# Kernel tuning notes

Hardware: AMD Instinct MI355X
Metric: run time of the kernel (lower is better)

## Reference

```python
import jax, jax.numpy as jnp
import numpy as np

L, H, E, DK, FF, V, BS = 6, 16, 1024, 64, 4096, 32000, 1024
B, T = 2, 1024
EPS = 1e-5


def _ln(x, g, b):
    mu = jnp.mean(x, axis=-1, keepdims=True)
    var = jnp.mean(jnp.square(x - mu), axis=-1, keepdims=True)
    return (x - mu) * jax.lax.rsqrt(var + EPS) * g + b


def setup_inputs() -> dict:
    key = jax.random.key(0)
    ks = jax.random.split(key, 12)
    s = 0.02
    return {
        'idx': jax.random.randint(ks[0], (B, T), 0, V),
        'emb': jax.random.normal(ks[1], (V, E), jnp.float32) * s,
        'pos': jax.random.normal(ks[2], (BS, E), jnp.float32) * s,
        'Wq': jax.random.normal(ks[3], (L, H, E, DK), jnp.float32) * s,
        'Wk': jax.random.normal(ks[4], (L, H, E, DK), jnp.float32) * s,
        'Wv': jax.random.normal(ks[5], (L, H, E, DK), jnp.float32) * s,
        'Wp': jax.random.normal(ks[6], (L, E, E), jnp.float32) * s,
        'bp': jnp.zeros((L, E), jnp.float32),
        'ln1_g': jnp.ones((L, E), jnp.float32),
        'ln1_b': jnp.zeros((L, E), jnp.float32),
        'ln2_g': jnp.ones((L, E), jnp.float32),
        'ln2_b': jnp.zeros((L, E), jnp.float32),
        'W1': jax.random.normal(ks[7], (L, E, FF), jnp.float32) * s,
        'b1': jnp.zeros((L, FF), jnp.float32),
        'W2': jax.random.normal(ks[8], (L, FF, E), jnp.float32) * s,
        'b2': jnp.zeros((L, E), jnp.float32),
        'lnf_g': jnp.ones((E,), jnp.float32),
        'lnf_b': jnp.zeros((E,), jnp.float32),
        'Wout': jax.random.normal(ks[9], (E, V), jnp.float32) * s,
        'bout': jnp.zeros((V,), jnp.float32),
    }


def reference(idx, emb, pos, Wq, Wk, Wv, Wp, bp, ln1_g, ln1_b, ln2_g, ln2_b,
              W1, b1, W2, b2, lnf_g, lnf_b, Wout, bout):
    Tcur = idx.shape[1]
    x = emb[idx] + pos[:Tcur]  # [B,T,E]
    # NOTE: original code scales by 1/sqrt(n_embd) (input dim), NOT 1/sqrt(d_k)
    scale = 1.0 / jnp.sqrt(jnp.float32(E))
    causal = jnp.tril(jnp.ones((Tcur, Tcur), bool))
    neg_inf = jnp.float32(-jnp.inf)
    for l in range(L):
        h = _ln(x, ln1_g[l], ln1_b[l])
        q = jnp.einsum('bte,hed->bhtd', h, Wq[l])
        k = jnp.einsum('bte,hed->bhtd', h, Wk[l])
        v = jnp.einsum('bte,hed->bhtd', h, Wv[l])
        scores = jnp.einsum('bhtd,bhsd->bhts', q, k) * scale
        scores = jnp.where(causal, scores, neg_inf)
        attn = jax.nn.softmax(scores, axis=-1)
        o = jnp.einsum('bhts,bhsd->bhtd', attn, v)
        o = o.transpose(0, 2, 1, 3).reshape(x.shape[0], Tcur, H * DK)
        x = x + o @ Wp[l] + bp[l]
        h = _ln(x, ln2_g[l], ln2_b[l])
        x = x + jax.nn.relu(h @ W1[l] + b1[l]) @ W2[l] + b2[l]
    x = _ln(x, lnf_g, lnf_b)
    logits = x @ Wout + bout  # [B,T,V]
    return logits
```

## Files before the change

### kernel.cpp

```cpp
#include <hip/hip_runtime.h>
#include <cstdio>
#include <cstdint>

typedef unsigned short u16;
typedef __bf16 bf16x8 __attribute__((ext_vector_type(8)));
typedef float f32x4 __attribute__((ext_vector_type(4)));

static const int EE = 1024;
static const int TT = 1024;
static const int BB = 2;
static const int NTOK = 2048;
static const int HH = 16;
static const int DK = 64;
static const int FF = 4096;
static const int VV = 32000;
static const int LL = 6;

__device__ __forceinline__ float bf2f(u16 u) {
  unsigned int i = ((unsigned int)u) << 16;
  float f; __builtin_memcpy(&f, &i, 4); return f;
}
__device__ __forceinline__ u16 f2bf(float f) {
  unsigned int i; __builtin_memcpy(&i, &f, 4);
  unsigned int r = i + 0x7fffu + ((i >> 16) & 1u);
  return (u16)(r >> 16);
}

__device__ __forceinline__ void gll16(const u16* g, u16* l) {
  __builtin_amdgcn_global_load_lds(
      (__attribute__((address_space(1))) void*)(uintptr_t)g,
      (__attribute__((address_space(3))) void*)l,
      16, 0, 0);
}

__global__ __launch_bounds__(256) void embed_k(const int* __restrict__ idx,
                                               const float* __restrict__ emb,
                                               const float* __restrict__ pos,
                                               float* __restrict__ x) {
  long i = (long)blockIdx.x * 256 + threadIdx.x;
  int n = (int)(i >> 10), e = (int)(i & 1023);
  int tok = idx[n];
  int t = n & (TT - 1);
  x[i] = emb[(long)tok * EE + e] + pos[(long)t * EE + e];
}

template <int NS>
__global__ __launch_bounds__(256) void ln_fused_k(float* __restrict__ x,
                                                  const float* __restrict__ part, long pstride,
                                                  const float* __restrict__ bias,
                                                  const float* __restrict__ g,
                                                  const float* __restrict__ b,
                                                  u16* __restrict__ out) {
  int row = blockIdx.x * 4 + (threadIdx.x >> 6);
  int lane = threadIdx.x & 63;
  long base = (long)row * EE;
  float v[16];
  float s = 0.f, s2 = 0.f;
#pragma unroll
  for (int j = 0; j < 16; j++) {
    int c = j * 64 + lane;
    float t = x[base + c];
    if constexpr (NS > 0) {
      t += bias[c];
#pragma unroll
      for (int p = 0; p < NS; p++) t += part[(long)p * pstride + base + c];
      x[base + c] = t;
    }
    v[j] = t; s += t; s2 += t * t;
  }
#pragma unroll
  for (int o = 32; o; o >>= 1) { s += __shfl_xor(s, o); s2 += __shfl_xor(s2, o); }
  float mu = s * (1.f / EE);
  float var = s2 * (1.f / EE) - mu * mu;
  float rs = rsqrtf(var + 1e-5f);
  u16* orow = out + base;
#pragma unroll
  for (int j = 0; j < 16; j++) {
    int c = j * 64 + lane;
    orow[c] = f2bf((v[j] - mu) * rs * g[c] + b[c]);
  }
}

__global__ __launch_bounds__(256) void pack_qkvT_k(const float* __restrict__ Wq,
                                                   const float* __restrict__ Wk,
                                                   const float* __restrict__ Wv,
                                                   u16* __restrict__ out) {
  int l = blockIdx.y;
  const float* Wq_l = Wq + (size_t)l * HH * EE * DK;
  const float* Wk_l = Wk + (size_t)l * HH * EE * DK;
  const float* Wv_l = Wv + (size_t)l * HH * EE * DK;
  u16* out_l = out + (size_t)l * 3 * EE * EE;
  long base = ((long)blockIdx.x * 256 + threadIdx.x) * 4;
  int c = (int)(base >> 10);
  int e0 = (int)(base & 1023);
  const float* W = (c < 1024) ? Wq_l : (c < 2048 ? Wk_l : Wv_l);
  int cm = c & 1023;
  int hh = cm >> 6, d = cm & 63;
#pragma unroll
  for (int i = 0; i < 4; i++) {
    int e = e0 + i;
    out_l[(long)c * EE + e] = f2bf(W[((long)hh * EE + e) * DK + d]);
  }
}

template <typename ST>
__global__ __launch_bounds__(256) void transpose_to_bf16(const ST* __restrict__ src,
                                                         long s_z1, long s_z2, int zmod, int ld_s,
                                                         u16* __restrict__ dst,
                                                         long d_z, int ld_d, int R, int C) {
  __shared__ u16 t[32][33];
  int z = blockIdx.z;
  const ST* S = src + (z / zmod) * s_z1 + (z % zmod) * s_z2;
  u16* D = dst + (long)z * d_z;
  int c0 = blockIdx.x * 32, r0 = blockIdx.y * 32;
  int lx = threadIdx.x & 31, ly = threadIdx.x >> 5;
#pragma unroll
  for (int i = 0; i < 4; i++) {
    int r = r0 + ly + i * 8;
    ST val = S[(long)r * ld_s + c0 + lx];
    if constexpr (sizeof(ST) == 4) t[ly + i * 8][lx] = f2bf((float)val);
    else t[ly + i * 8][lx] = (u16)val;
  }
  __syncthreads();
#pragma unroll
  for (int i = 0; i < 4; i++) {
    int c = c0 + ly + i * 8;
    D[(long)c * ld_d + r0 + lx] = t[lx][ly + i * 8];
  }
}

__global__ __launch_bounds__(256) void flash_attn_k(const u16* __restrict__ qkv,
                                                    const u16* __restrict__ vT,
                                                    u16* __restrict__ o) {
  __shared__ u16 Qs[64 * 72];
  __shared__ u16 Ks[2][64 * 72];
  __shared__ u16 Vs[2][64 * 72];
  __shared__ u16 Ps[4][16 * 72];

  int tid = threadIdx.x;
  int lane = tid & 63, w = tid >> 6;
  int fr = lane & 15, kg = lane >> 4;
  int z = blockIdx.y;
  int b = z >> 4, h = z & 15;
  const u16* qbase = qkv + (long)b * TT * 3072 + h * 64;
  const u16* kbase = qbase + 1024;
  const u16* vbase = vT + (long)z * DK * TT;
  const float scale = 0.03125f;

  for (int p = 0; p < 2; p++) {
    int jq = (p == 0) ? (int)blockIdx.x : 15 - (int)blockIdx.x;
    int q0 = jq * 64;
    int nt = jq + 1;
    if (p) __syncthreads();

    int4 kreg[2], vreg[2];
#pragma unroll
    for (int i = 0; i < 2; i++) {
      int c = i * 256 + tid, row = c >> 3, c8 = c & 7;
      *(int4*)&Qs[row * 72 + c8 * 8] = *(const int4*)(qbase + (long)(q0 + row) * 3072 + c8 * 8);
      kreg[i] = *(const int4*)(kbase + (long)row * 3072 + c8 * 8);
      vreg[i] = *(const int4*)(vbase + (long)row * TT + c8 * 8);
    }
#pragma unroll
    for (int i = 0; i < 2; i++) {
      int c = i * 256 + tid, row = c >> 3, c8 = c & 7;
      *(int4*)&Ks[0][row * 72 + c8 * 8] = kreg[i];
      *(int4*)&Vs[0][row * 72 + c8 * 8] = vreg[i];
    }
    __syncthreads();

    f32x4 zero = {0.f, 0.f, 0.f, 0.f};
    f32x4 acc_o[4];
    float m_i[4], l_i[4];
#pragma unroll
    for (int n = 0; n < 4; n++) acc_o[n] = zero;
#pragma unroll
    for (int r = 0; r < 4; r++) { m_i[r] = -1e30f; l_i[r] = 0.f; }

    for (int t = 0; t < nt; t++) {
      int cur = t & 1;
      int kv0 = t * 64;
      bool pf = (t + 1 < nt);
      if (pf) {
        int kvn = kv0 + 64;
#pragma unroll
        for (int i = 0; i < 2; i++) {
          int c = i * 256 + tid, row = c >> 3, c8 = c & 7;
          kreg[i] = *(const int4*)(kbase + (long)(kvn + row) * 3072 + c8 * 8);
          vreg[i] = *(const int4*)(vbase + (long)row * TT + kvn + c8 * 8);
        }
      }

      f32x4 s[4];
#pragma unroll
      for (int n = 0; n < 4; n++) s[n] = zero;
      {
        bf16x8 aq[2], bk[4][2];
#pragma unroll
        for (int kk = 0; kk < 2; kk++)
          aq[kk] = *(const bf16x8*)&Qs[(w * 16 + fr) * 72 + kk * 32 + kg * 8];
#pragma unroll
        for (int n = 0; n < 4; n++)
#pragma unroll
          for (int kk = 0; kk < 2; kk++)
            bk[n][kk] = *(const bf16x8*)&Ks[cur][(n * 16 + fr) * 72 + kk * 32 + kg * 8];
#pragma unroll
        for (int kk = 0; kk < 2; kk++)
#pragma unroll
          for (int n = 0; n < 4; n++)
            s[n] = __builtin_amdgcn_mfma_f32_16x16x32_bf16(aq[kk], bk[n][kk], s[n], 0, 0, 0);
      }

      float sv[4][4];
#pragma unroll
      for (int n = 0; n < 4; n++)
#pragma unroll
        for (int r = 0; r < 4; r++) {
          int qg = q0 + w * 16 + kg * 4 + r;
          int kgl = kv0 + n * 16 + fr;
          float val = s[n][r] * scale;
          sv[n][r] = (kgl > qg) ? -1e30f : val;
        }
#pragma unroll
      for (int r = 0; r < 4; r++) {
        float rm = fmaxf(fmaxf(sv[0][r], sv[1][r]), fmaxf(sv[2][r], sv[3][r]));
        rm = fmaxf(rm, __shfl_xor(rm, 1));
        rm = fmaxf(rm, __shfl_xor(rm, 2));
        rm = fmaxf(rm, __shfl_xor(rm, 4));
        rm = fmaxf(rm, __shfl_xor(rm, 8));
        float mn = fmaxf(m_i[r], rm);
        float f = __expf(m_i[r] - mn);
        m_i[r] = mn;
        float rs = 0.f;
#pragma unroll
        for (int n = 0; n < 4; n++) {
          float pv = __expf(sv[n][r] - mn);
          sv[n][r] = pv;
          rs += pv;
        }
        rs += __shfl_xor(rs, 1);
        rs += __shfl_xor(rs, 2);
        rs += __shfl_xor(rs, 4);
        rs += __shfl_xor(rs, 8);
        l_i[r] = l_i[r] * f + rs;
#pragma unroll
        for (int n = 0; n < 4; n++) acc_o[n][r] *= f;
      }
#pragma unroll
      for (int n = 0; n < 4; n++)
#pragma unroll
        for (int r = 0; r < 4; r++)
          Ps[w][(kg * 4 + r) * 72 + n * 16 + fr] = f2bf(sv[n][r]);

      {
        bf16x8 pa[2], bv[4][2];
#pragma unroll
        for (int kk = 0; kk < 2; kk++)
          pa[kk] = *(const bf16x8*)&Ps[w][fr * 72 + kk * 32 + kg * 8];
#pragma unroll
        for (int n = 0; n < 4; n++)
#pragma unroll
          for (int kk = 0; kk < 2; kk++)
            bv[n][kk] = *(const bf16x8*)&Vs[cur][(n * 16 + fr) * 72 + kk * 32 + kg * 8];
#pragma unroll
        for (int kk = 0; kk < 2; kk++)
#pragma unroll
          for (int n = 0; n < 4; n++)
            acc_o[n] = __builtin_amdgcn_mfma_f32_16x16x32_bf16(pa[kk], bv[n][kk], acc_o[n], 0, 0, 0);
      }

      if (pf) {
#pragma unroll
        for (int i = 0; i < 2; i++) {
          int c = i * 256 + tid, row = c >> 3, c8 = c & 7;
          *(int4*)&Ks[cur ^ 1][row * 72 + c8 * 8] = kreg[i];
          *(int4*)&Vs[cur ^ 1][row * 72 + c8 * 8] = vreg[i];
        }
      }
      __syncthreads();
    }

    u16* obase = o + ((long)b * TT + q0) * EE + h * 64;
#pragma unroll
    for (int r = 0; r < 4; r++) {
      float inv = 1.f / l_i[r];
      int qrow = w * 16 + kg * 4 + r;
#pragma unroll
      for (int n = 0; n < 4; n++)
        obase[(long)qrow * EE + n * 16 + fr] = f2bf(acc_o[n][r] * inv);
    }
  }
}

template <int EPI>
__global__ __launch_bounds__(256) void gemm_nt(
    const u16* __restrict__ A, const u16* __restrict__ BT, void* Cv,
    const float* __restrict__ bias,
    int Kc, int lda, int ldb, int ldc, long c_zs) {
  constexpr int BK = 64;
  __shared__ u16 As[2][128 * BK];
  __shared__ u16 Bs[2][128 * BK];

  int m0 = blockIdx.x * 128, n0 = blockIdx.y * 128;
  int z = blockIdx.z;
  int tid = threadIdx.x, lane = tid & 63, wave = tid >> 6;
  int wm = wave >> 1, wn = wave & 1;
  int fr = lane & 15, kg = lane >> 4;
  int xk0 = ((kg) ^ (fr & 7)) * 8;
  int xk1 = ((4 + kg) ^ (fr & 7)) * 8;
  int kbeg = z * Kc;

  auto STAGE = [&](int t, int b) {
    int k0 = kbeg + t * BK;
#pragma unroll
    for (int i = 0; i < 4; i++) {
      int c = i * 256 + tid, row = c >> 3;
      int ch = (c & 7) ^ (row & 7);
      gll16(A + (long)(m0 + row) * lda + k0 + ch * 8, &As[b][c * 8]);
      gll16(BT + (long)(n0 + row) * ldb + k0 + ch * 8, &Bs[b][c * 8]);
    }
  };

  f32x4 zero = {0.f, 0.f, 0.f, 0.f};
  f32x4 acc[4][4];
#pragma unroll
  for (int m = 0; m < 4; m++)
#pragma unroll
    for (int n = 0; n < 4; n++) acc[m][n] = zero;

  int NT = Kc / BK;
  STAGE(0, 0);
  if (NT > 1) STAGE(1, 1);

  for (int c = 0; c < NT; c++) {
    if (c + 1 < NT) asm volatile("s_waitcnt vmcnt(8)" ::: "memory");
    else            asm volatile("s_waitcnt vmcnt(0)" ::: "memory");
    __builtin_amdgcn_s_barrier();
    const u16* Ab = As[c & 1];
    const u16* Bb = Bs[c & 1];
#pragma unroll
    for (int kk = 0; kk < 2; kk++) {
      int xo = kk ? xk1 : xk0;
      bf16x8 af[4], bf[4];
#pragma unroll
      for (int m = 0; m < 4; m++)
        af[m] = *(const bf16x8*)&Ab[(wm * 64 + m * 16 + fr) * BK + xo];
#pragma unroll
      for (int n = 0; n < 4; n++)
        bf[n] = *(const bf16x8*)&Bb[(wn * 64 + n * 16 + fr) * BK + xo];
      __builtin_amdgcn_s_setprio(1);
#pragma unroll
      for (int m = 0; m < 4; m++)
#pragma unroll
        for (int n = 0; n < 4; n++)
          acc[m][n] = __builtin_amdgcn_mfma_f32_16x16x32_bf16(af[m], bf[n], acc[m][n], 0, 0, 0);
      __builtin_amdgcn_s_setprio(0);
    }
    __builtin_amdgcn_s_barrier();
    if (c + 2 < NT) STAGE(c + 2, c & 1);
  }

  u16* C16 = (u16*)Cv;
  float* C32 = (float*)Cv;
  long cb = (long)z * c_zs;
  int rowb = m0 + wm * 64, colb = n0 + wn * 64;
#pragma unroll
  for (int m = 0; m < 4; m++) {
#pragma unroll
    for (int n = 0; n < 4; n++) {
      int gc = colb + n * 16 + fr;
      float bv = 0.f;
      if (EPI == 1 || EPI == 2) bv = bias[gc];
#pragma unroll
      for (int r = 0; r < 4; r++) {
        int gr = rowb + m * 16 + kg * 4 + r;
        long ci = cb + (long)gr * ldc + gc;
        float val = acc[m][n][r];
        if (EPI == 0) C16[ci] = f2bf(val);
        else if (EPI == 1) C32[ci] = val + bv;
        else if (EPI == 2) C16[ci] = f2bf(fmaxf(val + bv, 0.f));
        else C32[ci] = val;
      }
    }
  }
}

__global__ __launch_bounds__(512) void gemm256_nt(
    const u16* __restrict__ A, const u16* __restrict__ BT,
    float* __restrict__ C, const float* __restrict__ bias,
    int K, int lda, int ldb, int ldc) {
  __shared__ u16 lds[2][2][256 * 64];

  int tid = threadIdx.x, lane = tid & 63, wave = tid >> 6;
  int wm = wave >> 2, wn = wave & 3;
  int fr = lane & 15, kg = lane >> 4;
  int m0 = blockIdx.x * 256, n0 = blockIdx.y * 256;

  auto STAGE = [&](int t, int b) {
    int k0 = t * 64;
#pragma unroll
    for (int r = 0; r < 4; r++) {
      int g = r * 512 + tid;
      int row = g >> 3, cl = (g & 7) ^ (row & 7);
      gll16(A + (long)(m0 + row) * lda + k0 + cl * 8, &lds[b][0][g * 8]);
    }
#pragma unroll
    for (int r = 0; r < 4; r++) {
      int g = r * 512 + tid;
      int row = g >> 3, cl = (g & 7) ^ (row & 7);
      gll16(BT + (long)(n0 + row) * ldb + k0 + cl * 8, &lds[b][1][g * 8]);
    }
  };

  f32x4 zero = {0.f, 0.f, 0.f, 0.f};
  f32x4 acc[8][4];
#pragma unroll
  for (int m = 0; m < 8; m++)
#pragma unroll
    for (int n = 0; n < 4; n++) acc[m][n] = zero;

  int NT = K / 64;
  STAGE(0, 0);
  if (NT > 1) STAGE(1, 1);

  for (int c = 0; c < NT; c++) {
    if (c + 1 < NT) asm volatile("s_waitcnt vmcnt(8)" ::: "memory");
    else            asm volatile("s_waitcnt vmcnt(0)" ::: "memory");
    __builtin_amdgcn_s_barrier();
    const u16* Ab = lds[c & 1][0];
    const u16* Bb = lds[c & 1][1];
#pragma unroll
    for (int ph = 0; ph < 4; ph++) {
      int mh = ph >> 1, nh = ph & 1;
      bf16x8 af[4][2], bf[2][2];
#pragma unroll
      for (int m = 0; m < 4; m++) {
        int row = wm * 128 + mh * 64 + m * 16 + fr;
#pragma unroll
        for (int kk = 0; kk < 2; kk++) {
          int cp = (kk * 4 + kg) ^ (row & 7);
          af[m][kk] = *(const bf16x8*)&Ab[row * 64 + cp * 8];
        }
      }
#pragma unroll
      for (int n = 0; n < 2; n++) {
        int row = wn * 64 + nh * 32 + n * 16 + fr;
#pragma unroll
        for (int kk = 0; kk < 2; kk++) {
          int cp = (kk * 4 + kg) ^ (row & 7);
          bf[n][kk] = *(const bf16x8*)&Bb[row * 64 + cp * 8];
        }
      }
      __builtin_amdgcn_s_setprio(1);
#pragma unroll
      for (int kk = 0; kk < 2; kk++)
#pragma unroll
        for (int m = 0; m < 4; m++)
#pragma unroll
          for (int n = 0; n < 2; n++)
            acc[mh * 4 + m][nh * 2 + n] = __builtin_amdgcn_mfma_f32_16x16x32_bf16(
                af[m][kk], bf[n][kk], acc[mh * 4 + m][nh * 2 + n], 0, 0, 0);
      __builtin_amdgcn_s_setprio(0);
    }
    __builtin_amdgcn_s_barrier();
    if (c + 2 < NT) STAGE(c + 2, c & 1);
  }

  int rowb = m0 + wm * 128, colb = n0 + wn * 64;
#pragma unroll
  for (int m = 0; m < 8; m++) {
#pragma unroll
    for (int n = 0; n < 4; n++) {
      int gc = colb + n * 16 + fr;
      float bv = bias[gc];
#pragma unroll
      for (int r = 0; r < 4; r++) {
        int gr = rowb + m * 16 + kg * 4 + r;
        __builtin_nontemporal_store(acc[m][n][r] + bv, &C[(long)gr * ldc + gc]);
      }
    }
  }
}

extern "C" void kernel_launch(void* const* d_in, const int* in_sizes, int n_in,
                              void* d_out, int out_size, void* d_ws, size_t ws_size,
                              hipStream_t stream) {
  const int*   idx  = (const int*)d_in[0];
  const float* emb  = (const float*)d_in[1];
  const float* pos  = (const float*)d_in[2];
  const float* Wq   = (const float*)d_in[3];
  const float* Wk   = (const float*)d_in[4];
  const float* Wv   = (const float*)d_in[5];
  const float* Wp   = (const float*)d_in[6];
  const float* bp   = (const float*)d_in[7];
  const float* ln1g = (const float*)d_in[8];
  const float* ln1b = (const float*)d_in[9];
  const float* ln2g = (const float*)d_in[10];
  const float* ln2b = (const float*)d_in[11];
  const float* W1   = (const float*)d_in[12];
  const float* b1   = (const float*)d_in[13];
  const float* W2   = (const float*)d_in[14];
  const float* b2   = (const float*)d_in[15];
  const float* lnfg = (const float*)d_in[16];
  const float* lnfb = (const float*)d_in[17];
  const float* Wout = (const float*)d_in[18];
  const float* bout = (const float*)d_in[19];

  char* w = (char*)d_ws;
  size_t off = 0;
  auto alloc = [&](size_t bytes) {
    void* p = w + off;
    off += (bytes + 255) & ~(size_t)255;
    return p;
  };
  float* x    = (float*)alloc((size_t)NTOK * EE * 4);
  u16* h      = (u16*)alloc((size_t)NTOK * EE * 2);
  u16* qkv    = (u16*)alloc((size_t)NTOK * 3 * EE * 2);
  u16* vT     = (u16*)alloc((size_t)BB * HH * DK * TT * 2);
  u16* big    = (u16*)alloc((size_t)VV * EE * 2);
  u16* o      = (u16*)alloc((size_t)NTOK * EE * 2);
  u16* mid    = (u16*)alloc((size_t)NTOK * FF * 2);
  u16* W1T    = (u16*)alloc((size_t)FF * EE * 2);
  u16* W2T    = (u16*)alloc((size_t)EE * FF * 2);
  float* pbuf = (float*)alloc((size_t)4 * NTOK * EE * 4);
  if (off > ws_size) {
    fprintf(stderr, "kernel_launch: ws too small, need %zu have %zu\n", off, ws_size);
    return;
  }
  u16* WqkvT_all = big;
  u16* WpT_all   = big + (size_t)6 * 3 * EE * EE;
  const long PS = (long)NTOK * EE;

  embed_k<<<NTOK * EE / 256, 256, 0, stream>>>(idx, emb, pos, x);
  pack_qkvT_k<<<dim3(3 * EE * EE / 1024, LL), 256, 0, stream>>>(Wq, Wk, Wv, WqkvT_all);
  transpose_to_bf16<float><<<dim3(32, 32, LL), 256, 0, stream>>>(
      Wp, (long)EE * EE, 0, 1, EE, WpT_all, (long)EE * EE, EE, EE, EE);

  for (int l = 0; l < LL; l++) {
    if (l == 0)
      ln_fused_k<0><<<NTOK / 4, 256, 0, stream>>>(x, nullptr, 0, nullptr,
                                                  ln1g, ln1b, h);
    else
      ln_fused_k<4><<<NTOK / 4, 256, 0, stream>>>(x, pbuf, PS, b2 + (l - 1) * EE,
                                                  ln1g + l * EE, ln1b + l * EE, h);
    gemm_nt<0><<<dim3(16, 24, 1), 256, 0, stream>>>(
        h, WqkvT_all + (size_t)l * 3 * EE * EE, qkv, nullptr,
        EE, EE, EE, 3 * EE, 0);
    transpose_to_bf16<u16><<<dim3(2, 32, 32), 256, 0, stream>>>(
        qkv + 2 * EE, (long)TT * 3 * EE, 64, 16, 3 * EE,
        vT, (long)DK * TT, TT, TT, DK);
    flash_attn_k<<<dim3(8, 32), 256, 0, stream>>>(qkv, vT, o);
    gemm_nt<4><<<dim3(16, 8, 2), 256, 0, stream>>>(
        o, WpT_all + (size_t)l * EE * EE, pbuf, nullptr,
        512, EE, EE, EE, PS);
    ln_fused_k<2><<<NTOK / 4, 256, 0, stream>>>(x, pbuf, PS, bp + l * EE,
                                                ln2g + l * EE, ln2b + l * EE, h);
    transpose_to_bf16<float><<<dim3(FF / 32, EE / 32, 1), 256, 0, stream>>>(
        W1 + (size_t)l * EE * FF, 0, 0, 1, FF, W1T, 0, EE, EE, FF);
    gemm_nt<2><<<dim3(16, 32, 1), 256, 0, stream>>>(
        h, W1T, mid, b1 + l * FF,
        EE, EE, EE, FF, 0);
    transpose_to_bf16<float><<<dim3(EE / 32, FF / 32, 1), 256, 0, stream>>>(
        W2 + (size_t)l * FF * EE, 0, 0, 1, EE, W2T, 0, FF, FF, EE);
    gemm_nt<4><<<dim3(16, 8, 4), 256, 0, stream>>>(
        mid, W2T, pbuf, nullptr,
        1024, FF, FF, EE, PS);
  }

  ln_fused_k<4><<<NTOK / 4, 256, 0, stream>>>(x, pbuf, PS, b2 + 5 * EE, lnfg, lnfb, h);
  u16* WoutT = big;
  transpose_to_bf16<float><<<dim3(VV / 32, EE / 32, 1), 256, 0, stream>>>(
      Wout, 0, 0, 1, VV, WoutT, 0, EE, EE, VV);
  gemm256_nt<<<dim3(NTOK / 256, VV / 256, 1), 512, 0, stream>>>(
      h, WoutT, (float*)d_out, bout, EE, EE, EE, VV);
}
```

Before: 1.338 ms.

## Use 256x128 tiles with triple-buffered LDS pipeline for logits GEMM

Replaces the double-buffered 256x256 output-projection GEMM with a 256x128-tile kernel that keeps three LDS stages. The prefetch for tile c+2 is now issued before the compute of tile c, with graded vmcnt waits, so loads overlap the MFMA work. The change also doubles the number of blocks, which gives better wave balance on the CUs, and swaps nontemporal output stores for normal stores. In exchange, the B tile is reused less per A tile and A is loaded twice as often overall.

```diff
diff --git a/kernel.cpp b/kernel.cpp
--- a/kernel.cpp
+++ b/kernel.cpp
@@ -385,53 +385,56 @@
   }
 }
 
-__global__ __launch_bounds__(512) void gemm256_nt(
+__global__ __launch_bounds__(512) void gemm256_3s(
     const u16* __restrict__ A, const u16* __restrict__ BT,
     float* __restrict__ C, const float* __restrict__ bias,
     int K, int lda, int ldb, int ldc) {
-  __shared__ u16 lds[2][2][256 * 64];
+  __shared__ u16 Abuf[3][256 * 64];
+  __shared__ u16 Bbuf[3][128 * 64];
 
   int tid = threadIdx.x, lane = tid & 63, wave = tid >> 6;
   int wm = wave >> 2, wn = wave & 3;
   int fr = lane & 15, kg = lane >> 4;
-  int m0 = blockIdx.x * 256, n0 = blockIdx.y * 256;
-
-  auto STAGE = [&](int t, int b) {
+  int m0 = blockIdx.x * 256, n0 = blockIdx.y * 128;
+
+  auto STAGE = [&](int t) {
+    int b = t % 3;
     int k0 = t * 64;
 #pragma unroll
     for (int r = 0; r < 4; r++) {
       int g = r * 512 + tid;
       int row = g >> 3, cl = (g & 7) ^ (row & 7);
-      gll16(A + (long)(m0 + row) * lda + k0 + cl * 8, &lds[b][0][g * 8]);
-    }
-#pragma unroll
-    for (int r = 0; r < 4; r++) {
+      gll16(A + (long)(m0 + row) * lda + k0 + cl * 8, &Abuf[b][g * 8]);
+    }
+#pragma unroll
+    for (int r = 0; r < 2; r++) {
       int g = r * 512 + tid;
       int row = g >> 3, cl = (g & 7) ^ (row & 7);
-      gll16(BT + (long)(n0 + row) * ldb + k0 + cl * 8, &lds[b][1][g * 8]);
+      gll16(BT + (long)(n0 + row) * ldb + k0 + cl * 8, &Bbuf[b][g * 8]);
     }
   };
 
   f32x4 zero = {0.f, 0.f, 0.f, 0.f};
-  f32x4 acc[8][4];
+  f32x4 acc[8][2];
 #pragma unroll
   for (int m = 0; m < 8; m++)
 #pragma unroll
-    for (int n = 0; n < 4; n++) acc[m][n] = zero;
+    for (int n = 0; n < 2; n++) acc[m][n] = zero;
 
   int NT = K / 64;
-  STAGE(0, 0);
-  if (NT > 1) STAGE(1, 1);
+  STAGE(0);
+  STAGE(1);
 
   for (int c = 0; c < NT; c++) {
-    if (c + 1 < NT) asm volatile("s_waitcnt vmcnt(8)" ::: "memory");
-    else            asm volatile("s_waitcnt vmcnt(0)" ::: "memory");
+    if (c + 2 < NT) STAGE(c + 2);
+    if (c + 3 <= NT)      asm volatile("s_waitcnt vmcnt(12)" ::: "memory");
+    else if (c + 2 == NT) asm volatile("s_waitcnt vmcnt(6)" ::: "memory");
+    else                  asm volatile("s_waitcnt vmcnt(0)" ::: "memory");
     __builtin_amdgcn_s_barrier();
-    const u16* Ab = lds[c & 1][0];
-    const u16* Bb = lds[c & 1][1];
-#pragma unroll
-    for (int ph = 0; ph < 4; ph++) {
-      int mh = ph >> 1, nh = ph & 1;
+    const u16* Ab = Abuf[c % 3];
+    const u16* Bb = Bbuf[c % 3];
+#pragma unroll
+    for (int mh = 0; mh < 2; mh++) {
       bf16x8 af[4][2], bf[2][2];
 #pragma unroll
       for (int m = 0; m < 4; m++) {
@@ -444,7 +447,7 @@
       }
 #pragma unroll
       for (int n = 0; n < 2; n++) {
-        int row = wn * 64 + nh * 32 + n * 16 + fr;
+        int row = wn * 32 + n * 16 + fr;
 #pragma unroll
         for (int kk = 0; kk < 2; kk++) {
           int cp = (kk * 4 + kg) ^ (row & 7);
@@ -458,25 +461,24 @@
         for (int m = 0; m < 4; m++)
 #pragma unroll
           for (int n = 0; n < 2; n++)
-            acc[mh * 4 + m][nh * 2 + n] = __builtin_amdgcn_mfma_f32_16x16x32_bf16(
-                af[m][kk], bf[n][kk], acc[mh * 4 + m][nh * 2 + n], 0, 0, 0);
+            acc[mh * 4 + m][n] = __builtin_amdgcn_mfma_f32_16x16x32_bf16(
+                af[m][kk], bf[n][kk], acc[mh * 4 + m][n], 0, 0, 0);
       __builtin_amdgcn_s_setprio(0);
     }
     __builtin_amdgcn_s_barrier();
-    if (c + 2 < NT) STAGE(c + 2, c & 1);
-  }
-
-  int rowb = m0 + wm * 128, colb = n0 + wn * 64;
+  }
+
+  int rowb = m0 + wm * 128, colb = n0 + wn * 32;
 #pragma unroll
   for (int m = 0; m < 8; m++) {
 #pragma unroll
-    for (int n = 0; n < 4; n++) {
+    for (int n = 0; n < 2; n++) {
       int gc = colb + n * 16 + fr;
       float bv = bias[gc];
 #pragma unroll
       for (int r = 0; r < 4; r++) {
-        int gr = rowb + m * 16 + kg * 4 + r;
-        __builtin_nontemporal_store(acc[m][n][r] + bv, &C[(long)gr * ldc + gc]);
+        int gr = rowb + (m >> 2) * 64 + (m & 3) * 16 + kg * 4 + r;
+        C[(long)gr * ldc + gc] = acc[m][n][r] + bv;
       }
     }
   }
@@ -571,6 +573,6 @@
   u16* WoutT = big;
   transpose_to_bf16<float><<<dim3(VV / 32, EE / 32, 1), 256, 0, stream>>>(
       Wout, 0, 0, 1, VV, WoutT, 0, EE, EE, VV);
-  gemm256_nt<<<dim3(NTOK / 256, VV / 256, 1), 512, 0, stream>>>(
+  gemm256_3s<<<dim3(NTOK / 256, VV / 128, 1), 512, 0, stream>>>(
       h, WoutT, (float*)d_out, bout, EE, EE, EE, VV);
 }
```

Measured after the change: 1.392 ms. +4.1%, slower.
